# Kernel tuning notes

Hardware: AMD Instinct MI355X
Metric: run time of the kernel (lower is better)

## Reference

```python
import jax, jax.numpy as jnp
import numpy as np

B, S, DIN, DOUT = 4, 2048, 4096, 4096

def setup_inputs() -> dict:
    key = jax.random.key(0)
    k1, k2, k3 = jax.random.split(key, 3)
    x = jax.random.normal(k1, (B, S, DIN), dtype=jnp.float32)
    # symmetric int8 quantized weights, [out_features, in_features]
    int_weight = jax.random.randint(k2, (DOUT, DIN), -128, 128, dtype=jnp.int32).astype(jnp.int8)
    w_scale = jnp.float32(0.01)  # per-tensor scale, zero-point = 0
    fp_bias = jax.random.normal(k3, (DOUT,), dtype=jnp.float32) * 0.01
    return {"x": x, "int_weight": int_weight, "w_scale": w_scale, "fp_bias": fp_bias}

def reference(x, int_weight, w_scale, fp_bias):
    # Dequantize weight: fp32 = int8 * scale (elementwise), then F.linear: x @ w.T + b
    w = int_weight.astype(jnp.float32) * w_scale  # [DOUT, DIN]
    out = jnp.einsum('bsi,oi->bso', x, w) + fp_bias
    return out
```

## Files before the change

### kernel.cpp

```cpp
#include <hip/hip_runtime.h>
#include <hip/hip_bf16.h>

typedef __attribute__((ext_vector_type(8))) short bf16x8;
typedef __attribute__((ext_vector_type(4))) float f32x4;
typedef __attribute__((ext_vector_type(4))) int i32x4;
typedef __attribute__((ext_vector_type(2))) unsigned int u32x2;
typedef __attribute__((ext_vector_type(4))) unsigned int u32x4;

__device__ __forceinline__ unsigned int f2bf(float f) {
    union { float f; unsigned int u; } v; v.f = f;
    unsigned int u = v.u;
    u += 0x7FFFu + ((u >> 16) & 1u);
    return u >> 16;
}

__device__ __forceinline__ void gl_lds16(const void* gptr, void* lptr) {
    __builtin_amdgcn_global_load_lds(
        (const __attribute__((address_space(1))) unsigned int*)gptr,
        (__attribute__((address_space(3))) unsigned int*)lptr, 16, 0, 0);
}

__global__ __launch_bounds__(256) void convert_x_kernel(
    const float* __restrict__ x, unsigned short* __restrict__ xb, long long n8)
{
    long long i = (long long)blockIdx.x * blockDim.x + threadIdx.x;
    const long long stride = (long long)gridDim.x * blockDim.x;
    for (; i < n8; i += stride) {
        const f32x4* p = (const f32x4*)(x + i * 8);
        f32x4 v0 = p[0], v1 = p[1];
        u32x4 q;
        q[0] = f2bf(v0[0]) | (f2bf(v0[1]) << 16);
        q[1] = f2bf(v0[2]) | (f2bf(v0[3]) << 16);
        q[2] = f2bf(v1[0]) | (f2bf(v1[1]) << 16);
        q[3] = f2bf(v1[2]) | (f2bf(v1[3]) << 16);
        *(u32x4*)(xb + i * 8) = q;
    }
}

__global__ __launch_bounds__(256) void convert_w_kernel(
    const int* __restrict__ w, unsigned short* __restrict__ wb, long long n8)
{
    long long i = (long long)blockIdx.x * blockDim.x + threadIdx.x;
    const long long stride = (long long)gridDim.x * blockDim.x;
    for (; i < n8; i += stride) {
        const i32x4* p = (const i32x4*)(w + i * 8);
        i32x4 v0 = p[0], v1 = p[1];
        u32x4 q;
        q[0] = f2bf((float)v0[0]) | (f2bf((float)v0[1]) << 16);
        q[1] = f2bf((float)v0[2]) | (f2bf((float)v0[3]) << 16);
        q[2] = f2bf((float)v1[0]) | (f2bf((float)v1[1]) << 16);
        q[3] = f2bf((float)v1[2]) | (f2bf((float)v1[3]) << 16);
        *(u32x4*)(wb + i * 8) = q;
    }
}

__global__ __launch_bounds__(512, 2) void gemm256_kernel(
    const unsigned short* __restrict__ A, const unsigned short* __restrict__ Bw,
    const float* __restrict__ wscale, const float* __restrict__ bias,
    float* __restrict__ out, int M, int N, int K)
{
    __shared__ unsigned char lds[131072];

    const int tid  = threadIdx.x;
    const int lane = tid & 63;
    const int wid  = tid >> 6;
    const int wr   = wid >> 2;
    const int wc   = wid & 3;

    const int ntn = N >> 8;
    const int nwg = gridDim.x;
    int bid = blockIdx.x;
    if ((nwg & 7) == 0) {
        const int cpx = nwg >> 3;
        bid = (bid & 7) * cpx + (bid >> 3);
    }
    const int bm = bid / ntn;
    const int bn = bid % ntn;
    const int NT = K >> 5 >> 1;

    const char* Abase = (const char*)(A  + (size_t)bm * 256 * K);
    const char* Bbase = (const char*)(Bw + (size_t)bn * 256 * K);
    const size_t rowb = (size_t)K * 2;

    const int s_row  = tid >> 3;
    const int s_colb = (((lane & 7) ^ (lane >> 3)) << 4);
    const int s_ldso = wid * 1024 + lane * 16;

    auto stage = [&](int kt, int c) {
        const char* Ag = Abase + (size_t)kt * 128;
        const char* Bg = Bbase + (size_t)kt * 128;
        char* Al = (char*)lds + (c << 16);
        char* Bl = Al + 32768;
#pragma unroll
        for (int q = 0; q < 4; ++q)
            gl_lds16(Ag + (size_t)(q * 64 + s_row) * rowb + s_colb,
                     Al + q * 8192 + s_ldso);
#pragma unroll
        for (int q = 0; q < 4; ++q)
            gl_lds16(Bg + (size_t)(q * 64 + s_row) * rowb + s_colb,
                     Bl + q * 8192 + s_ldso);
    };

    const int arow0 = (wr * 128 + (lane & 15)) * 128;
    const int brow0 = (wc * 64 + (lane & 15)) * 128;
    const int cswz0 = (((lane >> 4) * 16)      ) ^ ((lane & 7) << 4);
    const int cswz1 = (((lane >> 4) * 16) + 64 ) ^ ((lane & 7) << 4);

    f32x4 acc[8][4];
#pragma unroll
    for (int mi = 0; mi < 8; ++mi)
#pragma unroll
        for (int ni = 0; ni < 4; ++ni)
            acc[mi][ni] = (f32x4){0.f, 0.f, 0.f, 0.f};

    auto ldA = [&](const char* Al, int mh, int kk, bf16x8* a) {
        const int c = kk ? cswz1 : cswz0;
#pragma unroll
        for (int fm = 0; fm < 4; ++fm)
            a[fm] = *(const bf16x8*)(Al + arow0 + (mh * 64 + fm * 16) * 128 + c);
    };
    auto ldB = [&](const char* Bl, int kk, bf16x8* b) {
        const int c = kk ? cswz1 : cswz0;
#pragma unroll
        for (int fn = 0; fn < 4; ++fn)
            b[fn] = *(const bf16x8*)(Bl + brow0 + fn * 16 * 128 + c);
    };
    auto mm = [&](const bf16x8* a, const bf16x8* b, int mh) {
#pragma unroll
        for (int fm = 0; fm < 4; ++fm)
#pragma unroll
            for (int fn = 0; fn < 4; ++fn)
                acc[mh * 4 + fm][fn] = __builtin_amdgcn_mfma_f32_16x16x32_bf16(
                    a[fm], b[fn], acc[mh * 4 + fm][fn], 0, 0, 0);
    };

    stage(0, 0);
    asm volatile("s_waitcnt vmcnt(0)" ::: "memory");
    __builtin_amdgcn_sched_barrier(0);
    asm volatile("s_barrier" ::: "memory");

#pragma unroll 2
    for (int t = 0; t < NT; ++t) {
        const int c = t & 1;
        const char* Al = (const char*)lds + (c << 16);
        const char* Bl = Al + 32768;
        bf16x8 a[4], b[4];

        ldA(Al, 0, 0, a); ldB(Bl, 0, b);
        if (t + 1 < NT) stage(t + 1, c ^ 1);
        asm volatile("s_barrier" ::: "memory");
        __builtin_amdgcn_s_setprio(1); mm(a, b, 0); __builtin_amdgcn_s_setprio(0);
        asm volatile("s_barrier" ::: "memory");

        ldA(Al, 1, 0, a);
        asm volatile("s_barrier" ::: "memory");
        __builtin_amdgcn_s_setprio(1); mm(a, b, 1); __builtin_amdgcn_s_setprio(0);
        asm volatile("s_barrier" ::: "memory");

        ldA(Al, 0, 1, a); ldB(Bl, 1, b);
        asm volatile("s_barrier" ::: "memory");
        __builtin_amdgcn_s_setprio(1); mm(a, b, 0); __builtin_amdgcn_s_setprio(0);
        asm volatile("s_barrier" ::: "memory");

        ldA(Al, 1, 1, a);
        asm volatile("s_barrier" ::: "memory");
        __builtin_amdgcn_s_setprio(1); mm(a, b, 1); __builtin_amdgcn_s_setprio(0);
        asm volatile("s_waitcnt vmcnt(0) lgkmcnt(0)" ::: "memory");
        __builtin_amdgcn_sched_barrier(0);
        asm volatile("s_barrier" ::: "memory");
    }

    const float scale = *wscale;
    const int orow0 = bm * 256 + wr * 128 + ((lane >> 4) << 2);
    const int ocol0 = bn * 256 + wc * 64 + (lane & 15);
#pragma unroll
    for (int ni = 0; ni < 4; ++ni) {
        const int col = ocol0 + 16 * ni;
        const float bb = bias[col];
#pragma unroll
        for (int mi = 0; mi < 8; ++mi) {
            const int row0 = orow0 + (mi >> 2) * 64 + (mi & 3) * 16;
#pragma unroll
            for (int i = 0; i < 4; ++i)
                out[(size_t)(row0 + i) * N + col] = acc[mi][ni][i] * scale + bb;
        }
    }
}

__device__ __forceinline__ int swz(int row, int byte_in_row) {
    return row * 128 + (byte_in_row ^ ((row & 7) << 4));
}

__global__ __launch_bounds__(256) void qlinear_fused_kernel(
    const float* __restrict__ X, const int* __restrict__ W,
    const float* __restrict__ wscale, const float* __restrict__ bias,
    float* __restrict__ out, int M, int N, int K)
{
    __shared__ unsigned char smem[32768];

    const int t    = threadIdx.x;
    const int lane = t & 63;
    const int wid  = t >> 6;
    const int wr   = wid >> 1;
    const int wc   = wid & 1;

    const int ntn = N >> 7;
    const int bm  = blockIdx.x / ntn;
    const int bn  = blockIdx.x % ntn;
    const int NT  = K >> 6;

    const float* Ab = X + (size_t)bm * 128 * K;
    const int*   Bb = W + (size_t)bn * 128 * K;

    const int srow = t >> 4, sc4 = t & 15;

    f32x4 av[8];
    i32x4 bv[8];

    auto loadAB = [&](int kt) {
        const float* Ap = Ab + kt * 64 + sc4 * 4;
#pragma unroll
        for (int l = 0; l < 8; ++l)
            av[l] = *(const f32x4*)(Ap + (size_t)(srow + 16 * l) * K);
        const int* Bp = Bb + kt * 64 + sc4 * 4;
#pragma unroll
        for (int l = 0; l < 8; ++l)
            bv[l] = *(const i32x4*)(Bp + (size_t)(srow + 16 * l) * K);
    };

    auto writeAB = [&]() {
#pragma unroll
        for (int l = 0; l < 8; ++l) {
            const int row = srow + 16 * l;
            u32x2 pk;
            pk[0] = f2bf(av[l][0]) | (f2bf(av[l][1]) << 16);
            pk[1] = f2bf(av[l][2]) | (f2bf(av[l][3]) << 16);
            *(u32x2*)(smem + swz(row, sc4 * 8)) = pk;
        }
#pragma unroll
        for (int l = 0; l < 8; ++l) {
            const int row = srow + 16 * l;
            u32x2 pk;
            pk[0] = f2bf((float)bv[l][0]) | (f2bf((float)bv[l][1]) << 16);
            pk[1] = f2bf((float)bv[l][2]) | (f2bf((float)bv[l][3]) << 16);
            *(u32x2*)(smem + 16384 + swz(row, sc4 * 8)) = pk;
        }
    };

    f32x4 acc[4][4];
#pragma unroll
    for (int mi = 0; mi < 4; ++mi)
#pragma unroll
        for (int ni = 0; ni < 4; ++ni)
            acc[mi][ni] = (f32x4){0.f, 0.f, 0.f, 0.f};

    const int kbyte = (lane >> 4) * 16;
    const int afr   = wr * 64 + (lane & 15);
    const int bfr   = wc * 64 + (lane & 15);

    loadAB(0);

    for (int kt = 0; kt < NT; ++kt) {
        writeAB();
        __syncthreads();
        if (kt + 1 < NT) loadAB(kt + 1);
#pragma unroll
        for (int kk = 0; kk < 2; ++kk) {
            bf16x8 a[4], b[4];
#pragma unroll
            for (int mi = 0; mi < 4; ++mi)
                a[mi] = *(const bf16x8*)(smem + swz(afr + 16 * mi, kk * 64 + kbyte));
#pragma unroll
            for (int ni = 0; ni < 4; ++ni)
                b[ni] = *(const bf16x8*)(smem + 16384 + swz(bfr + 16 * ni, kk * 64 + kbyte));
#pragma unroll
            for (int mi = 0; mi < 4; ++mi)
#pragma unroll
                for (int ni = 0; ni < 4; ++ni)
                    acc[mi][ni] = __builtin_amdgcn_mfma_f32_16x16x32_bf16(
                        a[mi], b[ni], acc[mi][ni], 0, 0, 0);
        }
        __syncthreads();
    }

    const float scale = *wscale;
    const int orow0 = bm * 128 + wr * 64 + ((lane >> 4) << 2);
    const int ocol0 = bn * 128 + wc * 64 + (lane & 15);
#pragma unroll
    for (int ni = 0; ni < 4; ++ni) {
        const int col = ocol0 + 16 * ni;
        const float bb = bias[col];
#pragma unroll
        for (int mi = 0; mi < 4; ++mi) {
            const int row0 = orow0 + 16 * mi;
#pragma unroll
            for (int i = 0; i < 4; ++i)
                out[(size_t)(row0 + i) * N + col] = acc[mi][ni][i] * scale + bb;
        }
    }
}

extern "C" void kernel_launch(void* const* d_in, const int* in_sizes, int n_in,
                              void* d_out, int out_size, void* d_ws, size_t ws_size,
                              hipStream_t stream) {
    const float* x      = (const float*)d_in[0];
    const int*   w      = (const int*)d_in[1];
    const float* wscale = (const float*)d_in[2];
    const float* bias   = (const float*)d_in[3];
    float*       out    = (float*)d_out;

    const int DOUT = in_sizes[3];
    const int DIN  = in_sizes[1] / DOUT;
    const int M    = in_sizes[0] / DIN;

    const size_t xb_bytes = (size_t)M * DIN * 2;
    const size_t wb_bytes = (size_t)DOUT * DIN * 2;

    if (ws_size >= xb_bytes + wb_bytes && (M % 256) == 0 && (DOUT % 256) == 0) {
        unsigned short* xb = (unsigned short*)d_ws;
        unsigned short* wb = (unsigned short*)((char*)d_ws + xb_bytes);

        const long long nx8 = (long long)M * DIN / 8;
        const long long nw8 = (long long)DOUT * DIN / 8;
        convert_x_kernel<<<2048, 256, 0, stream>>>(x, xb, nx8);
        convert_w_kernel<<<2048, 256, 0, stream>>>(w, wb, nw8);

        dim3 grid((M / 256) * (DOUT / 256));
        gemm256_kernel<<<grid, 512, 0, stream>>>(xb, wb, wscale, bias, out, M, DOUT, DIN);
    } else {
        dim3 grid((M / 128) * (DOUT / 128));
        qlinear_fused_kernel<<<grid, 256, 0, stream>>>(x, w, wscale, bias, out, M, DOUT, DIN);
    }
}
```

Baseline: 316.7 us.

## Retile GEMM warps to 4x2 and stage A/B halves with finer-grained prefetch

Changes the 8-wave layout from 2x4 to 4x2, so each wave computes 64 rows by 128 columns. Global-to-LDS staging is split into half tiles spread across the four MFMA phases. A for step kt+2 is prefetched into the current buffer once it has been consumed, and the vmcnt waits are partial. The aim is to overlap memory loads with MFMA more evenly and to change the LDS read mix, at the cost of a more delicate buffer-reuse schedule with race risk.

```diff
diff --git a/kernel.cpp b/kernel.cpp
--- a/kernel.cpp
+++ b/kernel.cpp
@@ -64,8 +64,8 @@
     const int tid  = threadIdx.x;
     const int lane = tid & 63;
     const int wid  = tid >> 6;
-    const int wr   = wid >> 2;
-    const int wc   = wid & 3;
+    const int wr   = wid >> 1;
+    const int wc   = wid & 1;
 
     const int ntn = N >> 8;
     const int nwg = gridDim.x;
@@ -76,113 +76,134 @@
     }
     const int bm = bid / ntn;
     const int bn = bid % ntn;
-    const int NT = K >> 5 >> 1;
+    const int NT = K >> 6;
 
     const char* Abase = (const char*)(A  + (size_t)bm * 256 * K);
     const char* Bbase = (const char*)(Bw + (size_t)bn * 256 * K);
     const size_t rowb = (size_t)K * 2;
 
-    const int s_row  = tid >> 3;
     const int s_colb = (((lane & 7) ^ (lane >> 3)) << 4);
+    const int s_rsub = wid * 8 + (lane >> 3);
     const int s_ldso = wid * 1024 + lane * 16;
 
-    auto stage = [&](int kt, int c) {
-        const char* Ag = Abase + (size_t)kt * 128;
-        const char* Bg = Bbase + (size_t)kt * 128;
-        char* Al = (char*)lds + (c << 16);
-        char* Bl = Al + 32768;
-#pragma unroll
-        for (int q = 0; q < 4; ++q)
-            gl_lds16(Ag + (size_t)(q * 64 + s_row) * rowb + s_colb,
-                     Al + q * 8192 + s_ldso);
-#pragma unroll
-        for (int q = 0; q < 4; ++q)
-            gl_lds16(Bg + (size_t)(q * 64 + s_row) * rowb + s_colb,
-                     Bl + q * 8192 + s_ldso);
+    auto stageHalf = [&](const char* gRowBase, char* lhalf) {
+#pragma unroll
+        for (int q = 0; q < 2; ++q)
+            gl_lds16(gRowBase + (size_t)(q * 64 + s_rsub) * rowb + s_colb,
+                     lhalf + q * 8192 + s_ldso);
     };
-
-    const int arow0 = (wr * 128 + (lane & 15)) * 128;
-    const int brow0 = (wc * 64 + (lane & 15)) * 128;
-    const int cswz0 = (((lane >> 4) * 16)      ) ^ ((lane & 7) << 4);
-    const int cswz1 = (((lane >> 4) * 16) + 64 ) ^ ((lane & 7) << 4);
-
-    f32x4 acc[8][4];
-#pragma unroll
-    for (int mi = 0; mi < 8; ++mi)
-#pragma unroll
-        for (int ni = 0; ni < 4; ++ni)
+    auto Ag = [&](int kt, int h) { return Abase + (size_t)kt * 128 + (size_t)(h * 128) * rowb; };
+    auto Bg = [&](int kt, int h) { return Bbase + (size_t)kt * 128 + (size_t)(h * 128) * rowb; };
+
+    const int arow = (wr * 64  + (lane & 15)) * 128;
+    const int brow = (wc * 128 + (lane & 15)) * 128;
+    const int csw0 = (((lane >> 4) * 16))      ^ ((lane & 7) << 4);
+    const int csw1 = (((lane >> 4) * 16) + 64) ^ ((lane & 7) << 4);
+
+    f32x4 acc[4][8];
+#pragma unroll
+    for (int mi = 0; mi < 4; ++mi)
+#pragma unroll
+        for (int ni = 0; ni < 8; ++ni)
             acc[mi][ni] = (f32x4){0.f, 0.f, 0.f, 0.f};
 
-    auto ldA = [&](const char* Al, int mh, int kk, bf16x8* a) {
-        const int c = kk ? cswz1 : cswz0;
-#pragma unroll
-        for (int fm = 0; fm < 4; ++fm)
-            a[fm] = *(const bf16x8*)(Al + arow0 + (mh * 64 + fm * 16) * 128 + c);
-    };
-    auto ldB = [&](const char* Bl, int kk, bf16x8* b) {
-        const int c = kk ? cswz1 : cswz0;
-#pragma unroll
-        for (int fn = 0; fn < 4; ++fn)
-            b[fn] = *(const bf16x8*)(Bl + brow0 + fn * 16 * 128 + c);
-    };
-    auto mm = [&](const bf16x8* a, const bf16x8* b, int mh) {
-#pragma unroll
-        for (int fm = 0; fm < 4; ++fm)
-#pragma unroll
-            for (int fn = 0; fn < 4; ++fn)
-                acc[mh * 4 + fm][fn] = __builtin_amdgcn_mfma_f32_16x16x32_bf16(
-                    a[fm], b[fn], acc[mh * 4 + fm][fn], 0, 0, 0);
-    };
-
-    stage(0, 0);
-    asm volatile("s_waitcnt vmcnt(0)" ::: "memory");
+    stageHalf(Ag(0, 0), (char*)lds + 0);
+    stageHalf(Ag(0, 1), (char*)lds + 16384);
+    stageHalf(Bg(0, 0), (char*)lds + 32768);
+    stageHalf(Bg(0, 1), (char*)lds + 49152);
+    if (NT > 1) {
+        stageHalf(Ag(1, 0), (char*)lds + 65536);
+        stageHalf(Ag(1, 1), (char*)lds + 65536 + 16384);
+        asm volatile("s_waitcnt vmcnt(4)" ::: "memory");
+    } else {
+        asm volatile("s_waitcnt vmcnt(0)" ::: "memory");
+    }
     __builtin_amdgcn_sched_barrier(0);
     asm volatile("s_barrier" ::: "memory");
 
 #pragma unroll 2
-    for (int t = 0; t < NT; ++t) {
-        const int c = t & 1;
+    for (int kt = 0; kt < NT; ++kt) {
+        const int c = kt & 1;
         const char* Al = (const char*)lds + (c << 16);
         const char* Bl = Al + 32768;
-        bf16x8 a[4], b[4];
-
-        ldA(Al, 0, 0, a); ldB(Bl, 0, b);
-        if (t + 1 < NT) stage(t + 1, c ^ 1);
-        asm volatile("s_barrier" ::: "memory");
-        __builtin_amdgcn_s_setprio(1); mm(a, b, 0); __builtin_amdgcn_s_setprio(0);
-        asm volatile("s_barrier" ::: "memory");
-
-        ldA(Al, 1, 0, a);
-        asm volatile("s_barrier" ::: "memory");
-        __builtin_amdgcn_s_setprio(1); mm(a, b, 1); __builtin_amdgcn_s_setprio(0);
-        asm volatile("s_barrier" ::: "memory");
-
-        ldA(Al, 0, 1, a); ldB(Bl, 1, b);
-        asm volatile("s_barrier" ::: "memory");
-        __builtin_amdgcn_s_setprio(1); mm(a, b, 0); __builtin_amdgcn_s_setprio(0);
-        asm volatile("s_barrier" ::: "memory");
-
-        ldA(Al, 1, 1, a);
-        asm volatile("s_barrier" ::: "memory");
-        __builtin_amdgcn_s_setprio(1); mm(a, b, 1); __builtin_amdgcn_s_setprio(0);
-        asm volatile("s_waitcnt vmcnt(0) lgkmcnt(0)" ::: "memory");
+        char* nbuf = (char*)lds + ((c ^ 1) << 16);
+        char* cbuf = (char*)lds + (c << 16);
+        bf16x8 a0[4], a1[4], b[4], b2[4];
+
+#pragma unroll
+        for (int fm = 0; fm < 4; ++fm) a0[fm] = *(const bf16x8*)(Al + arow + fm * 16 * 128 + csw0);
+#pragma unroll
+        for (int fn = 0; fn < 4; ++fn) b[fn]  = *(const bf16x8*)(Bl + brow + fn * 16 * 128 + csw0);
+        if (kt + 1 < NT) stageHalf(Bg(kt + 1, 0), nbuf + 32768);
+        asm volatile("s_barrier" ::: "memory");
+        __builtin_amdgcn_s_setprio(1);
+#pragma unroll
+        for (int fm = 0; fm < 4; ++fm)
+#pragma unroll
+            for (int fn = 0; fn < 4; ++fn)
+                acc[fm][fn] = __builtin_amdgcn_mfma_f32_16x16x32_bf16(a0[fm], b[fn], acc[fm][fn], 0, 0, 0);
+        __builtin_amdgcn_s_setprio(0);
+        asm volatile("s_barrier" ::: "memory");
+
+#pragma unroll
+        for (int fm = 0; fm < 4; ++fm) a1[fm] = *(const bf16x8*)(Al + arow + fm * 16 * 128 + csw1);
+#pragma unroll
+        for (int fn = 0; fn < 4; ++fn) b2[fn] = *(const bf16x8*)(Bl + brow + (fn + 4) * 16 * 128 + csw0);
+        if (kt + 1 < NT) stageHalf(Bg(kt + 1, 1), nbuf + 49152);
+        asm volatile("s_barrier" ::: "memory");
+        __builtin_amdgcn_s_setprio(1);
+#pragma unroll
+        for (int fm = 0; fm < 4; ++fm)
+#pragma unroll
+            for (int fn = 0; fn < 4; ++fn)
+                acc[fm][fn + 4] = __builtin_amdgcn_mfma_f32_16x16x32_bf16(a0[fm], b2[fn], acc[fm][fn + 4], 0, 0, 0);
+        __builtin_amdgcn_s_setprio(0);
+        asm volatile("s_waitcnt lgkmcnt(0)" ::: "memory");
+        asm volatile("s_barrier" ::: "memory");
+
+#pragma unroll
+        for (int fn = 0; fn < 4; ++fn) b[fn]  = *(const bf16x8*)(Bl + brow + fn * 16 * 128 + csw1);
+#pragma unroll
+        for (int fn = 0; fn < 4; ++fn) b2[fn] = *(const bf16x8*)(Bl + brow + (fn + 4) * 16 * 128 + csw1);
+        if (kt + 2 < NT) stageHalf(Ag(kt + 2, 0), cbuf);
+        asm volatile("s_barrier" ::: "memory");
+        __builtin_amdgcn_s_setprio(1);
+#pragma unroll
+        for (int fm = 0; fm < 4; ++fm)
+#pragma unroll
+            for (int fn = 0; fn < 4; ++fn)
+                acc[fm][fn] = __builtin_amdgcn_mfma_f32_16x16x32_bf16(a1[fm], b[fn], acc[fm][fn], 0, 0, 0);
+        __builtin_amdgcn_s_setprio(0);
+        asm volatile("s_barrier" ::: "memory");
+
+        if (kt + 2 < NT) stageHalf(Ag(kt + 2, 1), cbuf + 16384);
+        asm volatile("s_barrier" ::: "memory");
+        __builtin_amdgcn_s_setprio(1);
+#pragma unroll
+        for (int fm = 0; fm < 4; ++fm)
+#pragma unroll
+            for (int fn = 0; fn < 4; ++fn)
+                acc[fm][fn + 4] = __builtin_amdgcn_mfma_f32_16x16x32_bf16(a1[fm], b2[fn], acc[fm][fn + 4], 0, 0, 0);
+        __builtin_amdgcn_s_setprio(0);
+        if (kt + 2 < NT) { asm volatile("s_waitcnt vmcnt(4)" ::: "memory"); }
+        else             { asm volatile("s_waitcnt vmcnt(0)" ::: "memory"); }
         __builtin_amdgcn_sched_barrier(0);
         asm volatile("s_barrier" ::: "memory");
     }
 
     const float scale = *wscale;
-    const int orow0 = bm * 256 + wr * 128 + ((lane >> 4) << 2);
-    const int ocol0 = bn * 256 + wc * 64 + (lane & 15);
-#pragma unroll
-    for (int ni = 0; ni < 4; ++ni) {
-        const int col = ocol0 + 16 * ni;
+    const int orow0 = bm * 256 + wr * 64  + ((lane >> 4) << 2);
+    const int ocol0 = bn * 256 + wc * 128 + (lane & 15);
+#pragma unroll
+    for (int fn = 0; fn < 8; ++fn) {
+        const int col = ocol0 + 16 * fn;
         const float bb = bias[col];
 #pragma unroll
-        for (int mi = 0; mi < 8; ++mi) {
-            const int row0 = orow0 + (mi >> 2) * 64 + (mi & 3) * 16;
+        for (int fm = 0; fm < 4; ++fm) {
+            const int row0 = orow0 + 16 * fm;
 #pragma unroll
             for (int i = 0; i < 4; ++i)
-                out[(size_t)(row0 + i) * N + col] = acc[mi][ni][i] * scale + bb;
+                out[(size_t)(row0 + i) * N + col] = acc[fm][fn][i] * scale + bb;
         }
     }
 }
```

Measured after the change: 292.7 us. -7.6%, faster.
